# Performance work log

Measured on AMD Instinct MI355X. Metric: run time of the kernel, lower is better.

Reference implementation:

```python
import jax, jax.numpy as jnp
import numpy as np
import math

EMBED = 256
HEADS = 8
HD = EMBED // HEADS  # 32
NB = 3               # n_behaviors
C = NB * NB + 1      # 10 behavior-pair classes
NUM_BUCKETS = 32
MAX_DIST = 40
EPS = 1e-12
B, L = 4, 512


def _rel_bucket(seq_len, num_buckets=NUM_BUCKETS, max_distance=MAX_DIST):
    """T5-style relative position buckets, matching RelativePositionBias._relative_position_bucket."""
    pos = jnp.arange(seq_len)
    relative_position = pos[None, :] - pos[:, None]  # k - q
    n = -relative_position
    nb = num_buckets // 2
    ret = (n < 0).astype(jnp.int32) * nb
    n = jnp.abs(n)
    max_exact = nb // 2
    is_small = n < max_exact
    nf = jnp.maximum(n, 1).astype(jnp.float32)  # clamp to avoid log(0); masked by is_small anyway
    val_large = max_exact + (jnp.log(nf / max_exact) / math.log(max_distance / max_exact) * (nb - max_exact)).astype(jnp.int32)
    val_large = jnp.minimum(val_large, nb - 1)
    return ret + jnp.where(is_small, n, val_large)


def setup_inputs() -> dict:
    key = jax.random.key(0)
    ks = jax.random.split(key, 12)
    s = 0.02
    return {
        "input_tensor": jax.random.normal(ks[0], (B, L, EMBED), jnp.float32),
        "attention_mask": jnp.zeros((B, 1, L, L), jnp.float32),
        "type_seq": jax.random.randint(ks[1], (B, L), 0, NB + 1),
        "Wq": jax.random.normal(ks[2], (NB + 1, EMBED, HEADS, HD), jnp.float32) * s,
        "Wk": jax.random.normal(ks[3], (NB + 1, EMBED, HEADS, HD), jnp.float32) * s,
        "Wv": jax.random.normal(ks[4], (NB + 1, EMBED, HEADS, HD), jnp.float32) * s,
        "W1": jax.random.normal(ks[5], (NB, HEADS, HD, HD), jnp.float32) * s,
        "alpha1": jax.random.normal(ks[6], (C, NB, HEADS), jnp.float32),
        "W2": jax.random.normal(ks[7], (NB, HEADS, HD, HD), jnp.float32) * s,
        "alpha2": jax.random.normal(ks[8], (C, NB, HEADS), jnp.float32),
        "rp_tables": jax.random.normal(ks[9], (C, NUM_BUCKETS, HEADS), jnp.float32) * s,
        "ln_gamma": jnp.ones((EMBED,), jnp.float32),
        "ln_beta": jnp.zeros((EMBED,), jnp.float32),
    }


def reference(input_tensor, attention_mask, type_seq, Wq, Wk, Wv, W1, alpha1, W2, alpha2, rp_tables, ln_gamma, ln_beta):
    bsz, seq_len, emb = input_tensor.shape
    ts = type_seq
    # behavior pair matrix: 0 if either side is padding, else (tq-1)*NB + tk in [1, NB^2]
    bm = ((ts[:, :, None] * ts[:, None, :]) != 0).astype(jnp.int32)
    bm = bm * ((ts[:, :, None] - 1) * NB + ts[:, None, :])  # [B,L,L]

    # --- relative position bias, gathered per behavior pair ---
    bucket = _rel_bucket(seq_len)                 # [L,L]
    vals = rp_tables[:, bucket, :]                # [C,L,L,H]
    qi = jnp.arange(seq_len)[None, :, None]
    ki = jnp.arange(seq_len)[None, None, :]
    bias = vals[bm, qi, ki]                       # [B,L,L,H] gathered along C per pair
    bias = jnp.transpose(bias, (0, 3, 1, 2))      # [B,H,L,L]

    # --- behavior-gated QKV ---
    oh = jax.nn.one_hot(ts, NB + 1, dtype=input_tensor.dtype)  # [B,L,NB+1]
    q = jnp.einsum('BLH,bHhd,BLb->BhLd', input_tensor, Wq, oh)
    k = jnp.einsum('BLH,bHhd,BLb->BhLd', input_tensor, Wk, oh)
    v = jnp.einsum('BLH,bHhd,BLb->BhLd', input_tensor, Wv, oh)

    # --- bilinear scores with per-pair mixing matrices ---
    W1_ = jnp.einsum('bhmn,Cbh->Chmn', W1, jax.nn.softmax(alpha1, axis=1))
    att_all = jnp.einsum('BhQm,Chmn,BhKn->BhQKC', q, W1_, k)  # [B,H,L,L,C]
    scores = jnp.take_along_axis(att_all, bm[:, None, :, :, None], axis=4)[..., 0]
    scores = scores * (1.0 / math.sqrt(HD)) + bias + attention_mask
    probs = jax.nn.softmax(scores, axis=-1)  # dropout=0.0 -> identity

    # --- behavior-mixed value aggregation ---
    W2_ = jnp.einsum('bhmn,Cbh->Chmn', W2, jax.nn.softmax(alpha2, axis=1))
    oh_bm = jax.nn.one_hot(bm, C, dtype=probs.dtype)          # [B,L,L,C]
    pC = probs[:, :, :, :, None] * oh_bm[:, None]             # [B,H,L,L,C]
    ctx = jnp.einsum('BhQKC,Chnm,BhKn->BhQm', pC, W2_, v)     # [B,H,L,d]

    ctx = jnp.transpose(ctx, (0, 2, 1, 3)).reshape(bsz, seq_len, emb)
    x = ctx + input_tensor  # out_dropout=0.0
    mu = jnp.mean(x, axis=-1, keepdims=True)
    var = jnp.mean(jnp.square(x - mu), axis=-1, keepdims=True)
    return (x - mu) / jnp.sqrt(var + EPS) * ln_gamma + ln_beta
```

## Files before the change

### kernel.cpp

```cpp
#include <hip/hip_runtime.h>
#include <math.h>

#define BB 4
#define LL 512
#define EMB 256
#define NH 8
#define HD 32
#define NB_ 3
#define CCN 10
#define NBKT 32
#define SCALE 0.17677669529663687f

typedef __bf16 bf16_t;
typedef __attribute__((ext_vector_type(8))) bf16_t bf16x8;
typedef __attribute__((ext_vector_type(4))) float f32x4;

__device__ __forceinline__ unsigned short f2b(float f) {
    unsigned int u = __float_as_uint(f);
    u += 0x7FFF + ((u >> 16) & 1);
    return (unsigned short)(u >> 16);
}
__device__ __forceinline__ float b2f(unsigned short s) {
    return __uint_as_float(((unsigned int)s) << 16);
}
__device__ __forceinline__ unsigned pack2(float a, float b) {
    return (unsigned)f2b(a) | ((unsigned)f2b(b) << 16);
}
__device__ __forceinline__ int bm_of(int tq, int tk) {
    return (tq * tk != 0) ? ((tq - 1) * 3 + tk) : 0;
}
__device__ __forceinline__ unsigned long long shfl_up64(unsigned long long v, int d) {
    unsigned lo = (unsigned)__shfl_up((int)(unsigned)v, d, 64);
    unsigned hi = (unsigned)__shfl_up((int)(v >> 32), d, 64);
    return (((unsigned long long)hi) << 32) | lo;
}

__device__ __forceinline__ void sort512(const int* __restrict__ tsb, int* spk,
                                        unsigned long long* wtll, int* msc, int tid) {
    int ty0 = tsb[2 * tid], ty1 = tsb[2 * tid + 1];
    unsigned long long pk = (1ULL << (16 * ty0)) + (1ULL << (16 * ty1));
    unsigned long long v = pk;
    int lane = tid & 63;
#pragma unroll
    for (int off = 1; off < 64; off <<= 1) {
        unsigned long long o = shfl_up64(v, off);
        if (lane >= off) v += o;
    }
    int w = tid >> 6;
    if (lane == 63) wtll[w] = v;
    __syncthreads();
    unsigned long long pre = 0, tot = 0;
#pragma unroll
    for (int i = 0; i < 4; i++) {
        unsigned long long xx = wtll[i];
        if (i < w) pre += xx;
        tot += xx;
    }
    v += pre;
    unsigned long long excl = v - pk;
    int c0 = (int)(tot & 0xFFFF), c1 = (int)((tot >> 16) & 0xFFFF);
    int c2 = (int)((tot >> 32) & 0xFFFF), c3 = (int)((tot >> 48) & 0xFFFF);
    int ub0 = 0, ub1 = c0, ub2 = c0 + c1, ub3 = c0 + c1 + c2;
    if (tid == 0) {
        int pc0 = (c0 + 31) & ~31, pc1 = (c1 + 31) & ~31, pc2 = (c2 + 31) & ~31, pc3 = (c3 + 31) & ~31;
        int pb1 = pc0, pb2 = pc0 + pc1, pb3 = pc0 + pc1 + pc2;
        msc[0] = 0;  msc[1] = pb1; msc[2] = pb2; msc[3] = pb3;
        msc[4] = ub0; msc[5] = ub1; msc[6] = ub2; msc[7] = ub3;
        msc[8] = c0; msc[9] = c1; msc[10] = c2; msc[11] = c3;
        msc[12] = (pb3 + pc3 + 63) & ~63;
    }
    int bases[4] = {ub0, ub1, ub2, ub3};
    int r0 = (int)((excl >> (16 * ty0)) & 0xFFFF);
    unsigned long long excl1 = excl + (1ULL << (16 * ty0));
    int r1 = (int)((excl1 >> (16 * ty1)) & 0xFFFF);
    spk[bases[ty0] + r0] = (ty0 << 16) | (2 * tid);
    spk[bases[ty1] + r1] = (ty1 << 16) | (2 * tid + 1);
    __syncthreads();
}

__device__ __forceinline__ void pad_lookup(const int* msc, int pos, int& real, int& upos, int& seg) {
    seg = (pos >= msc[1]) + (pos >= msc[2]) + (pos >= msc[3]);
    int r = pos - msc[seg];
    real = (r < msc[8 + seg]) ? 1 : 0;
    upos = msc[4 + seg] + r;
}

__global__ void k_pre(const float* __restrict__ A1, const float* __restrict__ W1,
                      const float* __restrict__ A2, const float* __restrict__ W2,
                      const float* __restrict__ Wq, const float* __restrict__ Wk, const float* __restrict__ Wv,
                      float* __restrict__ W1s, float* __restrict__ W2s,
                      unsigned short* __restrict__ W1Tb, unsigned short* __restrict__ W2Tb,
                      unsigned short* __restrict__ Wt) {
    __shared__ float cmb[32 * 33];
    __shared__ unsigned short ls[64 * 264];
    int g = blockIdx.x, tid = threadIdx.x;
    if (g < 160) {
        int idx = g;
        const float* alpha = (idx < 80) ? A1 : A2;
        const float* W     = (idx < 80) ? W1 : W2;
        float* Ws          = (idx < 80) ? W1s : W2s;
        unsigned short* WT = (idx < 80) ? W1Tb : W2Tb;
        idx %= 80;
        int cc = idx / NH, h = idx % NH;
        float a0 = alpha[cc * NB_ * NH + 0 * NH + h];
        float a1 = alpha[cc * NB_ * NH + 1 * NH + h];
        float a2 = alpha[cc * NB_ * NH + 2 * NH + h];
        float mx = fmaxf(a0, fmaxf(a1, a2));
        float e0 = __expf(a0 - mx), e1 = __expf(a1 - mx), e2 = __expf(a2 - mx);
        float inv = 1.0f / (e0 + e1 + e2);
        e0 *= inv; e1 *= inv; e2 *= inv;
        for (int i = tid; i < HD * HD; i += 256) {
            int m = i >> 5, n = i & 31;
            float acc = e0 * W[((0 * NH + h) * HD + m) * HD + n]
                      + e1 * W[((1 * NH + h) * HD + m) * HD + n]
                      + e2 * W[((2 * NH + h) * HD + m) * HD + n];
            cmb[m * 33 + n] = acc;
        }
        __syncthreads();
        for (int i = tid; i < HD * HD; i += 256) {
            int a = i >> 5, bq = i & 31;
            Ws[((cc * NH + h) * HD + a) * HD + bq] = cmb[a * 33 + bq];
            WT[((size_t)(cc * NH + h) * HD + a) * HD + bq] = f2b(cmb[bq * 33 + a]);
        }
        return;
    }
    int t = g - 160;
    int tw = t >> 2, ob = t & 3;
    int which = tw >> 2, ty = tw & 3;
    const float* src = ((which == 0) ? Wq : (which == 1) ? Wk : Wv) + (size_t)ty * EMB * EMB;
    int out0 = ob * 64;
    for (int it = 0; it < 16; it++) {
        int e = it * 16 + (tid >> 4);
        int o4 = (tid & 15) * 4;
        float4 v = *(const float4*)&src[(size_t)e * EMB + out0 + o4];
        ls[(o4 + 0) * 264 + e] = f2b(v.x);
        ls[(o4 + 1) * 264 + e] = f2b(v.y);
        ls[(o4 + 2) * 264 + e] = f2b(v.z);
        ls[(o4 + 3) * 264 + e] = f2b(v.w);
    }
    __syncthreads();
    int out = tid >> 2, ech = (tid & 3) * 8;
    unsigned short* dst = Wt + (size_t)tw * EMB * EMB + (size_t)(out0 + out) * EMB;
    const unsigned short* srcl = &ls[out * 264];
#pragma unroll
    for (int jj = 0; jj < 8; jj++)
        *(uint4*)&dst[ech + jj * 32] = *(const uint4*)&srcl[ech + jj * 32];
}

__global__ __launch_bounds__(256, 4) void k_qkv(
    const float* __restrict__ x, const int* __restrict__ ts,
    const unsigned short* __restrict__ Wt,
    float* __restrict__ qp, float* __restrict__ kp, float* __restrict__ vp) {
    __shared__ int spk[LL];
    __shared__ unsigned long long wtll[4];
    __shared__ int msc[16];
    __shared__ unsigned short xs[32 * 264];
    __shared__ unsigned short wt[128 * 72];

    int g = blockIdx.x, tid = threadIdx.x;
    int ns = g % 6, gb = g / 6;
    int b = gb >> 4, tb = gb & 15, i0 = tb * 32;
    int which = ns >> 1, nh = ns & 1;
    int wave = tid >> 6, lane = tid & 63, quad = lane >> 4, col = lane & 15;

    sort512(ts + b * LL, spk, wtll, msc, tid);

    {
        int tok = tid >> 3, e32 = (tid & 7) * 32;
        int tok_orig = spk[i0 + tok] & 0xFFFF;
        const float* src = &x[(size_t)(b * LL + tok_orig) * EMB + e32];
        unsigned short* dstl = &xs[tok * 264 + e32];
#pragma unroll
        for (int jj = 0; jj < 4; jj++) {
            float4 v0 = *(const float4*)&src[jj * 8];
            float4 v1 = *(const float4*)&src[jj * 8 + 4];
            uint4 w;
            w.x = pack2(v0.x, v0.y); w.y = pack2(v0.z, v0.w);
            w.z = pack2(v1.x, v1.y); w.w = pack2(v1.z, v1.w);
            *(uint4*)&dstl[jj * 8] = w;
        }
    }
    int t_start = spk[i0] >> 16, t_end = spk[i0 + 31] >> 16;
    float* outp = (which == 0) ? qp : (which == 1) ? kp : vp;

    for (int ty = t_start; ty <= t_end; ty++) {
        f32x4 acc[2][2];
#pragma unroll
        for (int mt = 0; mt < 2; mt++)
#pragma unroll
            for (int nt = 0; nt < 2; nt++) acc[mt][nt] = (f32x4){0.f, 0.f, 0.f, 0.f};
        const unsigned short* wsrc = Wt + (size_t)(which * 4 + ty) * EMB * EMB + (size_t)(nh * 128) * EMB;
        for (int c = 0; c < 4; c++) {
            {
                int outloc = tid >> 1, e32 = (tid & 1) * 32;
                const unsigned short* srcw = &wsrc[(size_t)outloc * EMB + c * 64 + e32];
                unsigned short* dstw = &wt[outloc * 72 + e32];
#pragma unroll
                for (int jj = 0; jj < 4; jj++)
                    *(uint4*)&dstw[jj * 8] = *(const uint4*)&srcw[jj * 8];
            }
            __syncthreads();
#pragma unroll
            for (int kk = 0; kk < 2; kk++) {
                bf16x8 a0 = *(const bf16x8*)&xs[(0 * 16 + col) * 264 + c * 64 + kk * 32 + quad * 8];
                bf16x8 a1 = *(const bf16x8*)&xs[(1 * 16 + col) * 264 + c * 64 + kk * 32 + quad * 8];
                bf16x8 b0 = *(const bf16x8*)&wt[((wave * 2 + 0) * 16 + col) * 72 + kk * 32 + quad * 8];
                bf16x8 b1 = *(const bf16x8*)&wt[((wave * 2 + 1) * 16 + col) * 72 + kk * 32 + quad * 8];
                acc[0][0] = __builtin_amdgcn_mfma_f32_16x16x32_bf16(a0, b0, acc[0][0], 0, 0, 0);
                acc[0][1] = __builtin_amdgcn_mfma_f32_16x16x32_bf16(a0, b1, acc[0][1], 0, 0, 0);
                acc[1][0] = __builtin_amdgcn_mfma_f32_16x16x32_bf16(a1, b0, acc[1][0], 0, 0, 0);
                acc[1][1] = __builtin_amdgcn_mfma_f32_16x16x32_bf16(a1, b1, acc[1][1], 0, 0, 0);
            }
            __syncthreads();
        }
#pragma unroll
        for (int mt = 0; mt < 2; mt++)
#pragma unroll
            for (int r = 0; r < 4; r++) {
                int tokloc = mt * 16 + quad * 4 + r;
                int tty = spk[i0 + tokloc] >> 16;
                if (tty != ty) continue;
#pragma unroll
                for (int nt = 0; nt < 2; nt++) {
                    int n = nh * 128 + (wave * 2 + nt) * 16 + col;
                    int h = n >> 5, d = n & 31;
                    outp[((size_t)(b * NH + h) * LL + i0 + tokloc) * HD + d] = acc[mt][nt][r];
                }
            }
    }
}

#define SCP 648
#define OFF_UN   20736
#define OFF_QTB  29184
#define OFF_KPAD 33536
#define OFF_TBL  36096
#define OFF_RPL  37120
#define OFF_WT   38400
#define OFF_QOR  38432
#define OFF_QTY  38496
#define OFF_INV  38560
#define OFF_MSC  38624
#define SM_TOTAL 38688
__global__ __launch_bounds__(256, 4) void k_attn(
    const float* __restrict__ qp, const float* __restrict__ kp, const float* __restrict__ vp,
    const int* __restrict__ ts, const float* __restrict__ rp, const float* __restrict__ am,
    const float* __restrict__ W1s, const float* __restrict__ W2s,
    const unsigned short* __restrict__ W1Tb, const unsigned short* __restrict__ W2Tb,
    float* __restrict__ ctx) {
    __shared__ __align__(16) char smem[SM_TOTAL];
    unsigned short* scu = (unsigned short*)smem;
    int*   spk  = (int*)smem;
    unsigned short* qstb = (unsigned short*)(smem + OFF_UN);
    unsigned short* kbuf = (unsigned short*)(smem + OFF_UN);
    unsigned short* vt   = (unsigned short*)(smem + OFF_UN);
    float* sb   = (float*)(smem + OFF_UN);
    unsigned short* qtb = (unsigned short*)(smem + OFF_QTB);
    unsigned short* sbb = (unsigned short*)(smem + OFF_QTB);
    int*   kpad = (int*)(smem + OFF_KPAD);
    short* tbl  = (short*)(smem + OFF_TBL);
    float* rp_l = (float*)(smem + OFF_RPL);
    unsigned long long* wtll = (unsigned long long*)(smem + OFF_WT);
    int*   qor_l = (int*)(smem + OFF_QOR);
    int*   qty_l = (int*)(smem + OFF_QTY);
    float* inv_l = (float*)(smem + OFF_INV);
    int*   msc   = (int*)(smem + OFF_MSC);

    int blk = blockIdx.x;
    int b = blk >> 8, h = (blk >> 5) & 7, q16 = blk & 31;
    int i0q = q16 * 16;
    int tid = threadIdx.x;
    int wave = tid >> 6, lane = tid & 63, quad = lane >> 4, col = lane & 15;
    int bh = b * NH + h;

    for (int d = tid; d < LL; d += 256) {
        int v;
        if (d < 8) v = d;
        else {
            double r = log((double)d / 8.0) / log(5.0);
            v = 8 + (int)(r * 8.0);
            if (v > 15) v = 15;
        }
        tbl[d] = (short)v;
    }
    for (int i = tid; i < CCN * NBKT; i += 256) rp_l[i] = rp[i * NH + h];

    sort512(ts + b * LL, spk, wtll, msc, tid);

    int KT = msc[12];
    if (tid < 16) {
        int v = spk[i0q + tid];
        qor_l[tid] = v & 0xFFFF; qty_l[tid] = v >> 16;
    }
    for (int pos = tid; pos < KT; pos += 256) {
        int real, upos, seg;
        pad_lookup(msc, pos, real, upos, seg);
        kpad[pos] = real ? spk[upos] : ((seg << 16) | 0xFFFF);
    }
    {
        int q = tid >> 4, m2 = (tid & 15) * 2;
        const float* src = &qp[((size_t)bh * LL + i0q + q) * HD + m2];
        ((unsigned*)qstb)[q * 20 + (tid & 15)] = pack2(src[0], src[1]);
    }
    __syncthreads();

    int qor_r[4], qty_r[4];
#pragma unroll
    for (int r = 0; r < 4; r++) { qor_r[r] = qor_l[quad * 4 + r]; qty_r[r] = qty_l[quad * 4 + r]; }
    bool uniq = (qty_l[0] == qty_l[15]);
    int tqu = qty_l[0];

    if (uniq) {
#pragma unroll
        for (int it = 0; it < 2; it++) {
            int t8 = wave * 2 + it;
            int tk = t8 >> 1, nhf = t8 & 1;
            int bmv = bm_of(tqu, tk);
            bf16x8 a = *(const bf16x8*)&qstb[col * 40 + quad * 8];
            bf16x8 bb = *(const bf16x8*)&W1Tb[((size_t)(bmv * NH + h) * HD + nhf * 16 + col) * HD + quad * 8];
            f32x4 d = {0.f, 0.f, 0.f, 0.f};
            d = __builtin_amdgcn_mfma_f32_16x16x32_bf16(a, bb, d, 0, 0, 0);
#pragma unroll
            for (int r = 0; r < 4; r++)
                qtb[(quad * 4 + r) * 136 + tk * 32 + nhf * 16 + col] = f2b(d[r]);
        }
    } else {
        for (int i = tid; i < 16 * 128; i += 256) {
            int q = i >> 7, r = i & 127, tk = r >> 5, n = r & 31;
            int bmv = bm_of(qty_l[q], tk);
            const float* wb = &W1s[((bmv * NH + h) * HD) * HD + n];
            float acc = 0.f;
#pragma unroll
            for (int m = 0; m < HD; m++) acc += b2f(qstb[q * 40 + m]) * wb[m * HD];
            qtb[q * 136 + tk * 32 + n] = f2b(acc);
        }
    }
    __syncthreads();

    const float* amb = am + (size_t)b * LL * LL;
    for (int kt0 = 0; kt0 < KT; kt0 += 64) {
        {
            int kk = tid >> 2, m8 = (tid & 3) * 8;
            int real, upos, seg;
            pad_lookup(msc, kt0 + kk, real, upos, seg);
            uint4 w = make_uint4(0, 0, 0, 0);
            if (real) {
                const float4* src = (const float4*)&kp[((size_t)bh * LL + upos) * HD + m8];
                float4 v0 = src[0], v1 = src[1];
                w.x = pack2(v0.x, v0.y); w.y = pack2(v0.z, v0.w);
                w.z = pack2(v1.x, v1.y); w.w = pack2(v1.z, v1.w);
            }
            *(uint4*)&kbuf[kk * 40 + m8] = w;
        }
        __syncthreads();
        {
            int kb = kt0 + wave * 16;
            int tk = kpad[kb] >> 16;
            bf16x8 a = *(const bf16x8*)&qtb[col * 136 + tk * 32 + quad * 8];
            bf16x8 bfr = *(const bf16x8*)&kbuf[(wave * 16 + col) * 40 + quad * 8];
            f32x4 d = {0.f, 0.f, 0.f, 0.f};
            d = __builtin_amdgcn_mfma_f32_16x16x32_bf16(a, bfr, d, 0, 0, 0);
            int kpi = kb + col;
            int kv = kpad[kpi];
            int ko = kv & 0xFFFF;
            if (ko == 0xFFFF) {
#pragma unroll
                for (int r = 0; r < 4; r++) scu[(quad * 4 + r) * SCP + kpi] = 0xFF80;
            } else {
                int tkk = kv >> 16;
#pragma unroll
                for (int r = 0; r < 4; r++) {
                    int q = quad * 4 + r;
                    int qo = qor_r[r];
                    int dd = qo - ko;
                    int ad = dd < 0 ? -dd : dd;
                    int bk = (dd < 0 ? 16 : 0) + (int)tbl[ad];
                    float bias = rp_l[bm_of(qty_r[r], tkk) * NBKT + bk];
                    float mval = amb[(size_t)qo * LL + ko];
                    scu[q * SCP + kpi] = f2b(d[r] * SCALE + bias + mval);
                }
            }
        }
        __syncthreads();
    }

    {
        int gq = tid >> 4, t16 = tid & 15;
        float mx = -1e30f;
        for (int kk = t16; kk < KT; kk += 16) mx = fmaxf(mx, b2f(scu[gq * SCP + kk]));
#pragma unroll
        for (int off = 1; off < 16; off <<= 1) mx = fmaxf(mx, __shfl_xor(mx, off, 16));
        float sum = 0.f;
        for (int kk = t16; kk < KT; kk += 16) {
            int idx = gq * SCP + kk;
            float e = __expf(b2f(scu[idx]) - mx);
            scu[idx] = f2b(e); sum += e;
        }
#pragma unroll
        for (int off = 1; off < 16; off <<= 1) sum += __shfl_xor(sum, off, 16);
        if (t16 == 0) inv_l[gq] = 1.0f / sum;
    }
    __syncthreads();

    f32x4 accv[4][2];
#pragma unroll
    for (int t = 0; t < 4; t++)
#pragma unroll
        for (int hh = 0; hh < 2; hh++) accv[t][hh] = (f32x4){0.f, 0.f, 0.f, 0.f};

    for (int kt0 = 0; kt0 < KT; kt0 += 64) {
        {
            int kk = tid >> 2, n8 = (tid & 3) * 8;
            int real, upos, seg;
            pad_lookup(msc, kt0 + kk, real, upos, seg);
            float vv[8] = {0, 0, 0, 0, 0, 0, 0, 0};
            if (real) {
                const float4* src = (const float4*)&vp[((size_t)bh * LL + upos) * HD + n8];
                float4 v0 = src[0], v1 = src[1];
                vv[0] = v0.x; vv[1] = v0.y; vv[2] = v0.z; vv[3] = v0.w;
                vv[4] = v1.x; vv[5] = v1.y; vv[6] = v1.z; vv[7] = v1.w;
            }
#pragma unroll
            for (int i = 0; i < 8; i++) {
                int n = n8 + i;
                int ph = ((n & 3) << 3) | (n >> 2);
                vt[ph * 72 + kk] = f2b(vv[i]);
            }
        }
        __syncthreads();
        int c = kt0 >> 6;
        int g0 = 2 * c;
        int pc = ((col & 3) << 3) | (col >> 2);
#pragma unroll
        for (int gl = 0; gl < 2; gl++) {
            int g = g0 + gl;
            if ((g & 3) != wave) continue;
            int loc = gl * 32;
            int tk = kpad[kt0 + loc] >> 16;
            bf16x8 a = *(const bf16x8*)&scu[col * SCP + kt0 + loc + quad * 8];
            bf16x8 b0 = *(const bf16x8*)&vt[pc * 72 + loc + quad * 8];
            bf16x8 b1 = *(const bf16x8*)&vt[(pc + 4) * 72 + loc + quad * 8];
            if (tk == 0) {
                accv[0][0] = __builtin_amdgcn_mfma_f32_16x16x32_bf16(a, b0, accv[0][0], 0, 0, 0);
                accv[0][1] = __builtin_amdgcn_mfma_f32_16x16x32_bf16(a, b1, accv[0][1], 0, 0, 0);
            } else if (tk == 1) {
                accv[1][0] = __builtin_amdgcn_mfma_f32_16x16x32_bf16(a, b0, accv[1][0], 0, 0, 0);
                accv[1][1] = __builtin_amdgcn_mfma_f32_16x16x32_bf16(a, b1, accv[1][1], 0, 0, 0);
            } else if (tk == 2) {
                accv[2][0] = __builtin_amdgcn_mfma_f32_16x16x32_bf16(a, b0, accv[2][0], 0, 0, 0);
                accv[2][1] = __builtin_amdgcn_mfma_f32_16x16x32_bf16(a, b1, accv[2][1], 0, 0, 0);
            } else {
                accv[3][0] = __builtin_amdgcn_mfma_f32_16x16x32_bf16(a, b0, accv[3][0], 0, 0, 0);
                accv[3][1] = __builtin_amdgcn_mfma_f32_16x16x32_bf16(a, b1, accv[3][1], 0, 0, 0);
            }
        }
        __syncthreads();
    }

#pragma unroll
    for (int w = 0; w < 4; w++) {
        if (wave == w) {
#pragma unroll
            for (int t = 0; t < 4; t++)
#pragma unroll
                for (int hh = 0; hh < 2; hh++)
#pragma unroll
                    for (int r = 0; r < 4; r++) {
                        int q = quad * 4 + r;
                        int n = col + 16 * hh;
                        float val = accv[t][hh][r];
                        if (w == 0) {
                            sb[q * 132 + t * 32 + n] = val;
                        } else if (w < 3) {
                            sb[q * 132 + t * 32 + n] += val;
                        } else {
                            float fin = sb[q * 132 + t * 32 + n] + val;
                            sb[q * 132 + t * 32 + n] = fin;
                            sbb[q * 136 + t * 32 + n] = f2b(fin);
                        }
                    }
        }
        __syncthreads();
    }

    if (uniq) {
        if (wave < 2) {
            int mhf = wave;
            f32x4 d = {0.f, 0.f, 0.f, 0.f};
#pragma unroll
            for (int tk = 0; tk < 4; tk++) {
                int bmv = bm_of(tqu, tk);
                bf16x8 a = *(const bf16x8*)&sbb[col * 136 + tk * 32 + quad * 8];
                bf16x8 bb = *(const bf16x8*)&W2Tb[((size_t)(bmv * NH + h) * HD + mhf * 16 + col) * HD + quad * 8];
                d = __builtin_amdgcn_mfma_f32_16x16x32_bf16(a, bb, d, 0, 0, 0);
            }
#pragma unroll
            for (int r = 0; r < 4; r++) {
                int q = quad * 4 + r;
                ctx[((size_t)(b * LL + qor_l[q])) * EMB + h * HD + mhf * 16 + col] = d[r] * inv_l[q];
            }
        }
    } else {
        int m = tid & 31, qq = tid >> 5;
#pragma unroll
        for (int rep = 0; rep < 2; rep++) {
            int qi = qq + 8 * rep;
            int tq = qty_l[qi];
            float acc = 0.f;
#pragma unroll
            for (int tk2 = 0; tk2 < 4; tk2++) {
                int bmv = bm_of(tq, tk2);
                const float* wb = &W2s[((bmv * NH + h) * HD) * HD + m];
                const float* sbp = &sb[qi * 132 + tk2 * 32];
                for (int n = 0; n < HD; n++) acc += sbp[n] * wb[n * HD];
            }
            int qo = qor_l[qi];
            ctx[((size_t)(b * LL + qo)) * EMB + h * HD + m] = acc * inv_l[qi];
        }
    }
}

__global__ void k_ln(const float* __restrict__ ctx, const float* __restrict__ x,
                     const float* __restrict__ gamma, const float* __restrict__ beta,
                     float* __restrict__ out) {
    __shared__ float red[8];
    __shared__ float red2[8];
    int blk = blockIdx.x;
    int b = blk >> 9, l = blk & 511;
    int j = threadIdx.x;
    size_t base = ((size_t)(b * LL + l)) * EMB;
    float v = ctx[base + j] + x[base + j];
    float s = v, s2 = v * v;
    for (int off = 32; off > 0; off >>= 1) { s += __shfl_down(s, off, 64); s2 += __shfl_down(s2, off, 64); }
    int wid = j >> 6;
    if ((j & 63) == 0) { red[wid] = s; red2[wid] = s2; }
    __syncthreads();
    if (j == 0) {
        float ts_ = 0, ts2 = 0;
        for (int w = 0; w < 4; w++) { ts_ += red[w]; ts2 += red2[w]; }
        red[4] = ts_; red2[4] = ts2;
    }
    __syncthreads();
    float mu = red[4] / (float)EMB;
    float var = red2[4] / (float)EMB - mu * mu;
    float r = rsqrtf(var + 1e-12f);
    out[base + j] = (v - mu) * r * gamma[j] + beta[j];
}

extern "C" void kernel_launch(void* const* d_in, const int* in_sizes, int n_in,
                              void* d_out, int out_size, void* d_ws, size_t ws_size,
                              hipStream_t stream) {
    const float* x  = (const float*)d_in[0];
    const float* am = (const float*)d_in[1];
    const int*   ts = (const int*)d_in[2];
    const float* Wq = (const float*)d_in[3];
    const float* Wk = (const float*)d_in[4];
    const float* Wv = (const float*)d_in[5];
    const float* W1 = (const float*)d_in[6];
    const float* a1 = (const float*)d_in[7];
    const float* W2 = (const float*)d_in[8];
    const float* a2 = (const float*)d_in[9];
    const float* rp = (const float*)d_in[10];
    const float* g  = (const float*)d_in[11];
    const float* be = (const float*)d_in[12];
    float* out = (float*)d_out;

    float* ws  = (float*)d_ws;
    float* W1s = ws;
    float* W2s = ws + 81920;
    unsigned short* W1Tb = (unsigned short*)(ws + 163840);
    unsigned short* W2Tb = (unsigned short*)(ws + 204800);
    float* qp  = ws + 245760;
    float* kp  = qp + BB * NH * LL * HD;
    float* vp  = kp + BB * NH * LL * HD;
    float* ctx = vp + BB * NH * LL * HD;
    unsigned short* Wt = (unsigned short*)ctx;

    hipLaunchKernelGGL(k_pre, dim3(208), dim3(256), 0, stream,
                       a1, W1, a2, W2, Wq, Wk, Wv, W1s, W2s, W1Tb, W2Tb, Wt);
    hipLaunchKernelGGL(k_qkv, dim3(384), dim3(256), 0, stream, x, ts, Wt, qp, kp, vp);
    hipLaunchKernelGGL(k_attn, dim3(BB * NH * 32), dim3(256), 0, stream,
                       qp, kp, vp, ts, rp, am, W1s, W2s, W1Tb, W2Tb, ctx);
    hipLaunchKernelGGL(k_ln, dim3(BB * LL), dim3(256), 0, stream, ctx, x, g, be, out);
}
```

Baseline: 139.9 us.

## Store Q/K/V as bf16, skip zero attention mask, drop LDS staging

Q, K and V projections are now written as bf16 instead of fp32, which halves their global traffic and removes repacking in the attention kernel. The prep kernel gets 256 extra blocks that scan the attention mask and set a device flag when any value is nonzero, so the attention kernel can skip mask loads when the mask is all zero. The QKV GEMM now loads A fragments into registers and B directly from global, removing LDS staging and barriers. The score loop is restructured so each wave handles its own key tiles without per-tile block syncs, and fully padded tiles are skipped. Padded-key metadata is packed into a single int per key.

```diff
diff --git a/kernel.cpp b/kernel.cpp
--- a/kernel.cpp
+++ b/kernel.cpp
@@ -88,9 +88,10 @@
 __global__ void k_pre(const float* __restrict__ A1, const float* __restrict__ W1,
                       const float* __restrict__ A2, const float* __restrict__ W2,
                       const float* __restrict__ Wq, const float* __restrict__ Wk, const float* __restrict__ Wv,
+                      const float* __restrict__ am,
                       float* __restrict__ W1s, float* __restrict__ W2s,
                       unsigned short* __restrict__ W1Tb, unsigned short* __restrict__ W2Tb,
-                      unsigned short* __restrict__ Wt) {
+                      unsigned short* __restrict__ Wt, int* __restrict__ mflag) {
     __shared__ float cmb[32 * 33];
     __shared__ unsigned short ls[64 * 264];
     int g = blockIdx.x, tid = threadIdx.x;
@@ -124,38 +125,50 @@
         }
         return;
     }
-    int t = g - 160;
-    int tw = t >> 2, ob = t & 3;
-    int which = tw >> 2, ty = tw & 3;
-    const float* src = ((which == 0) ? Wq : (which == 1) ? Wk : Wv) + (size_t)ty * EMB * EMB;
-    int out0 = ob * 64;
-    for (int it = 0; it < 16; it++) {
-        int e = it * 16 + (tid >> 4);
-        int o4 = (tid & 15) * 4;
-        float4 v = *(const float4*)&src[(size_t)e * EMB + out0 + o4];
-        ls[(o4 + 0) * 264 + e] = f2b(v.x);
-        ls[(o4 + 1) * 264 + e] = f2b(v.y);
-        ls[(o4 + 2) * 264 + e] = f2b(v.z);
-        ls[(o4 + 3) * 264 + e] = f2b(v.w);
-    }
-    __syncthreads();
-    int out = tid >> 2, ech = (tid & 3) * 8;
-    unsigned short* dst = Wt + (size_t)tw * EMB * EMB + (size_t)(out0 + out) * EMB;
-    const unsigned short* srcl = &ls[out * 264];
-#pragma unroll
-    for (int jj = 0; jj < 8; jj++)
-        *(uint4*)&dst[ech + jj * 32] = *(const uint4*)&srcl[ech + jj * 32];
+    if (g < 208) {
+        int t = g - 160;
+        int tw = t >> 2, ob = t & 3;
+        int which = tw >> 2, ty = tw & 3;
+        const float* src = ((which == 0) ? Wq : (which == 1) ? Wk : Wv) + (size_t)ty * EMB * EMB;
+        int out0 = ob * 64;
+        for (int it = 0; it < 16; it++) {
+            int e = it * 16 + (tid >> 4);
+            int o4 = (tid & 15) * 4;
+            float4 v = *(const float4*)&src[(size_t)e * EMB + out0 + o4];
+            ls[(o4 + 0) * 264 + e] = f2b(v.x);
+            ls[(o4 + 1) * 264 + e] = f2b(v.y);
+            ls[(o4 + 2) * 264 + e] = f2b(v.z);
+            ls[(o4 + 3) * 264 + e] = f2b(v.w);
+        }
+        __syncthreads();
+        int out = tid >> 2, ech = (tid & 3) * 8;
+        unsigned short* dst = Wt + (size_t)tw * EMB * EMB + (size_t)(out0 + out) * EMB;
+        const unsigned short* srcl = &ls[out * 264];
+#pragma unroll
+        for (int jj = 0; jj < 8; jj++)
+            *(uint4*)&dst[ech + jj * 32] = *(const uint4*)&srcl[ech + jj * 32];
+        return;
+    }
+    {
+        int idx = g - 208;
+        const uint4* p = (const uint4*)am + (size_t)idx * 1024;
+        unsigned o = 0;
+#pragma unroll
+        for (int j = 0; j < 4; j++) {
+            uint4 v = p[tid + j * 256];
+            o |= v.x | v.y | v.z | v.w;
+        }
+        if (o) atomicOr(mflag, 1);
+    }
 }
 
 __global__ __launch_bounds__(256, 4) void k_qkv(
     const float* __restrict__ x, const int* __restrict__ ts,
     const unsigned short* __restrict__ Wt,
-    float* __restrict__ qp, float* __restrict__ kp, float* __restrict__ vp) {
+    unsigned short* __restrict__ qp, unsigned short* __restrict__ kp, unsigned short* __restrict__ vp) {
     __shared__ int spk[LL];
     __shared__ unsigned long long wtll[4];
     __shared__ int msc[16];
-    __shared__ unsigned short xs[32 * 264];
-    __shared__ unsigned short wt[128 * 72];
 
     int g = blockIdx.x, tid = threadIdx.x;
     int ns = g % 6, gb = g / 6;
@@ -165,23 +178,23 @@
 
     sort512(ts + b * LL, spk, wtll, msc, tid);
 
-    {
-        int tok = tid >> 3, e32 = (tid & 7) * 32;
-        int tok_orig = spk[i0 + tok] & 0xFFFF;
-        const float* src = &x[(size_t)(b * LL + tok_orig) * EMB + e32];
-        unsigned short* dstl = &xs[tok * 264 + e32];
-#pragma unroll
-        for (int jj = 0; jj < 4; jj++) {
-            float4 v0 = *(const float4*)&src[jj * 8];
-            float4 v1 = *(const float4*)&src[jj * 8 + 4];
-            uint4 w;
-            w.x = pack2(v0.x, v0.y); w.y = pack2(v0.z, v0.w);
-            w.z = pack2(v1.x, v1.y); w.w = pack2(v1.z, v1.w);
-            *(uint4*)&dstl[jj * 8] = w;
+    bf16x8 afr[2][8];
+#pragma unroll
+    for (int mt = 0; mt < 2; mt++) {
+        int orig = spk[i0 + mt * 16 + col] & 0xFFFF;
+        const float* xr = &x[(size_t)(b * LL + orig) * EMB];
+#pragma unroll
+        for (int kc = 0; kc < 8; kc++) {
+            float4 v0 = *(const float4*)&xr[kc * 32 + quad * 8];
+            float4 v1 = *(const float4*)&xr[kc * 32 + quad * 8 + 4];
+            uint4 up;
+            up.x = pack2(v0.x, v0.y); up.y = pack2(v0.z, v0.w);
+            up.z = pack2(v1.x, v1.y); up.w = pack2(v1.z, v1.w);
+            afr[mt][kc] = *(bf16x8*)&up;
         }
     }
     int t_start = spk[i0] >> 16, t_end = spk[i0 + 31] >> 16;
-    float* outp = (which == 0) ? qp : (which == 1) ? kp : vp;
+    unsigned short* outp = (which == 0) ? qp : (which == 1) ? kp : vp;
 
     for (int ty = t_start; ty <= t_end; ty++) {
         f32x4 acc[2][2];
@@ -190,28 +203,16 @@
 #pragma unroll
             for (int nt = 0; nt < 2; nt++) acc[mt][nt] = (f32x4){0.f, 0.f, 0.f, 0.f};
         const unsigned short* wsrc = Wt + (size_t)(which * 4 + ty) * EMB * EMB + (size_t)(nh * 128) * EMB;
-        for (int c = 0; c < 4; c++) {
-            {
-                int outloc = tid >> 1, e32 = (tid & 1) * 32;
-                const unsigned short* srcw = &wsrc[(size_t)outloc * EMB + c * 64 + e32];
-                unsigned short* dstw = &wt[outloc * 72 + e32];
-#pragma unroll
-                for (int jj = 0; jj < 4; jj++)
-                    *(uint4*)&dstw[jj * 8] = *(const uint4*)&srcw[jj * 8];
-            }
-            __syncthreads();
-#pragma unroll
-            for (int kk = 0; kk < 2; kk++) {
-                bf16x8 a0 = *(const bf16x8*)&xs[(0 * 16 + col) * 264 + c * 64 + kk * 32 + quad * 8];
-                bf16x8 a1 = *(const bf16x8*)&xs[(1 * 16 + col) * 264 + c * 64 + kk * 32 + quad * 8];
-                bf16x8 b0 = *(const bf16x8*)&wt[((wave * 2 + 0) * 16 + col) * 72 + kk * 32 + quad * 8];
-                bf16x8 b1 = *(const bf16x8*)&wt[((wave * 2 + 1) * 16 + col) * 72 + kk * 32 + quad * 8];
-                acc[0][0] = __builtin_amdgcn_mfma_f32_16x16x32_bf16(a0, b0, acc[0][0], 0, 0, 0);
-                acc[0][1] = __builtin_amdgcn_mfma_f32_16x16x32_bf16(a0, b1, acc[0][1], 0, 0, 0);
-                acc[1][0] = __builtin_amdgcn_mfma_f32_16x16x32_bf16(a1, b0, acc[1][0], 0, 0, 0);
-                acc[1][1] = __builtin_amdgcn_mfma_f32_16x16x32_bf16(a1, b1, acc[1][1], 0, 0, 0);
-            }
-            __syncthreads();
+        const unsigned short* w0 = &wsrc[(size_t)((wave * 2 + 0) * 16 + col) * EMB + quad * 8];
+        const unsigned short* w1 = &wsrc[(size_t)((wave * 2 + 1) * 16 + col) * EMB + quad * 8];
+#pragma unroll
+        for (int kc = 0; kc < 8; kc++) {
+            bf16x8 b0 = *(const bf16x8*)&w0[kc * 32];
+            bf16x8 b1 = *(const bf16x8*)&w1[kc * 32];
+            acc[0][0] = __builtin_amdgcn_mfma_f32_16x16x32_bf16(afr[0][kc], b0, acc[0][0], 0, 0, 0);
+            acc[0][1] = __builtin_amdgcn_mfma_f32_16x16x32_bf16(afr[0][kc], b1, acc[0][1], 0, 0, 0);
+            acc[1][0] = __builtin_amdgcn_mfma_f32_16x16x32_bf16(afr[1][kc], b0, acc[1][0], 0, 0, 0);
+            acc[1][1] = __builtin_amdgcn_mfma_f32_16x16x32_bf16(afr[1][kc], b1, acc[1][1], 0, 0, 0);
         }
 #pragma unroll
         for (int mt = 0; mt < 2; mt++)
@@ -224,7 +225,7 @@
                 for (int nt = 0; nt < 2; nt++) {
                     int n = nh * 128 + (wave * 2 + nt) * 16 + col;
                     int h = n >> 5, d = n & 31;
-                    outp[((size_t)(b * NH + h) * LL + i0 + tokloc) * HD + d] = acc[mt][nt][r];
+                    outp[((size_t)(b * NH + h) * LL + i0 + tokloc) * HD + d] = f2b(acc[mt][nt][r]);
                 }
             }
     }
@@ -243,16 +244,16 @@
 #define OFF_MSC  38624
 #define SM_TOTAL 38688
 __global__ __launch_bounds__(256, 4) void k_attn(
-    const float* __restrict__ qp, const float* __restrict__ kp, const float* __restrict__ vp,
+    const unsigned short* __restrict__ qp, const unsigned short* __restrict__ kp,
+    const unsigned short* __restrict__ vp,
     const int* __restrict__ ts, const float* __restrict__ rp, const float* __restrict__ am,
     const float* __restrict__ W1s, const float* __restrict__ W2s,
     const unsigned short* __restrict__ W1Tb, const unsigned short* __restrict__ W2Tb,
-    float* __restrict__ ctx) {
+    const int* __restrict__ mflag, float* __restrict__ ctx) {
     __shared__ __align__(16) char smem[SM_TOTAL];
     unsigned short* scu = (unsigned short*)smem;
     int*   spk  = (int*)smem;
     unsigned short* qstb = (unsigned short*)(smem + OFF_UN);
-    unsigned short* kbuf = (unsigned short*)(smem + OFF_UN);
     unsigned short* vt   = (unsigned short*)(smem + OFF_UN);
     float* sb   = (float*)(smem + OFF_UN);
     unsigned short* qtb = (unsigned short*)(smem + OFF_QTB);
@@ -272,6 +273,7 @@
     int tid = threadIdx.x;
     int wave = tid >> 6, lane = tid & 63, quad = lane >> 4, col = lane & 15;
     int bh = b * NH + h;
+    int mz = (mflag[0] == 0);
 
     for (int d = tid; d < LL; d += 256) {
         int v;
@@ -295,12 +297,13 @@
     for (int pos = tid; pos < KT; pos += 256) {
         int real, upos, seg;
         pad_lookup(msc, pos, real, upos, seg);
-        kpad[pos] = real ? spk[upos] : ((seg << 16) | 0xFFFF);
+        int orig = real ? (spk[upos] & 0xFFFF) : 0x3FF;
+        kpad[pos] = (seg << 20) | ((real ? upos : 0) << 10) | orig;
     }
     {
         int q = tid >> 4, m2 = (tid & 15) * 2;
-        const float* src = &qp[((size_t)bh * LL + i0q + q) * HD + m2];
-        ((unsigned*)qstb)[q * 20 + (tid & 15)] = pack2(src[0], src[1]);
+        ((unsigned*)qstb)[q * 20 + (tid & 15)] =
+            *(const unsigned*)&qp[((size_t)bh * LL + i0q + q) * HD + m2];
     }
     __syncthreads();
 
@@ -338,51 +341,45 @@
     __syncthreads();
 
     const float* amb = am + (size_t)b * LL * LL;
-    for (int kt0 = 0; kt0 < KT; kt0 += 64) {
-        {
-            int kk = tid >> 2, m8 = (tid & 3) * 8;
-            int real, upos, seg;
-            pad_lookup(msc, kt0 + kk, real, upos, seg);
-            uint4 w = make_uint4(0, 0, 0, 0);
-            if (real) {
-                const float4* src = (const float4*)&kp[((size_t)bh * LL + upos) * HD + m8];
-                float4 v0 = src[0], v1 = src[1];
-                w.x = pack2(v0.x, v0.y); w.y = pack2(v0.z, v0.w);
-                w.z = pack2(v1.x, v1.y); w.w = pack2(v1.z, v1.w);
-            }
-            *(uint4*)&kbuf[kk * 40 + m8] = w;
-        }
-        __syncthreads();
-        {
-            int kb = kt0 + wave * 16;
-            int tk = kpad[kb] >> 16;
-            bf16x8 a = *(const bf16x8*)&qtb[col * 136 + tk * 32 + quad * 8];
-            bf16x8 bfr = *(const bf16x8*)&kbuf[(wave * 16 + col) * 40 + quad * 8];
-            f32x4 d = {0.f, 0.f, 0.f, 0.f};
-            d = __builtin_amdgcn_mfma_f32_16x16x32_bf16(a, bfr, d, 0, 0, 0);
-            int kpi = kb + col;
-            int kv = kpad[kpi];
-            int ko = kv & 0xFFFF;
-            if (ko == 0xFFFF) {
-#pragma unroll
-                for (int r = 0; r < 4; r++) scu[(quad * 4 + r) * SCP + kpi] = 0xFF80;
-            } else {
-                int tkk = kv >> 16;
-#pragma unroll
-                for (int r = 0; r < 4; r++) {
-                    int q = quad * 4 + r;
-                    int qo = qor_r[r];
-                    int dd = qo - ko;
-                    int ad = dd < 0 ? -dd : dd;
-                    int bk = (dd < 0 ? 16 : 0) + (int)tbl[ad];
-                    float bias = rp_l[bm_of(qty_r[r], tkk) * NBKT + bk];
-                    float mval = amb[(size_t)qo * LL + ko];
-                    scu[q * SCP + kpi] = f2b(d[r] * SCALE + bias + mval);
-                }
-            }
-        }
-        __syncthreads();
-    }
+    int ntiles = KT >> 4;
+    for (int tile = wave; tile < ntiles; tile += 4) {
+        int kb = tile * 16;
+        int kv0 = kpad[kb];
+        if ((kv0 & 0x3FF) == 0x3FF) {
+#pragma unroll
+            for (int r = 0; r < 4; r++) scu[(quad * 4 + r) * SCP + kb + col] = 0xFF80;
+            continue;
+        }
+        int tkt = kv0 >> 20;
+        int kpi = kb + col;
+        int kv = kpad[kpi];
+        int ko = kv & 0x3FF;
+        int upos = (kv >> 10) & 0x3FF;
+        bool real = (ko != 0x3FF);
+        bf16x8 bfr;
+        if (real) bfr = *(const bf16x8*)&kp[((size_t)bh * LL + upos) * HD + quad * 8];
+        else { uint4 z = make_uint4(0, 0, 0, 0); bfr = *(bf16x8*)&z; }
+        bf16x8 a = *(const bf16x8*)&qtb[col * 136 + tkt * 32 + quad * 8];
+        f32x4 d = {0.f, 0.f, 0.f, 0.f};
+        d = __builtin_amdgcn_mfma_f32_16x16x32_bf16(a, bfr, d, 0, 0, 0);
+        if (!real) {
+#pragma unroll
+            for (int r = 0; r < 4; r++) scu[(quad * 4 + r) * SCP + kpi] = 0xFF80;
+        } else {
+#pragma unroll
+            for (int r = 0; r < 4; r++) {
+                int q = quad * 4 + r;
+                int qo = qor_r[r];
+                int dd = qo - ko;
+                int ad = dd < 0 ? -dd : dd;
+                int bk = (dd < 0 ? 16 : 0) + (int)tbl[ad];
+                float sv = d[r] * SCALE + rp_l[bm_of(qty_r[r], tkt) * NBKT + bk];
+                if (!mz) sv += amb[(size_t)qo * LL + ko];
+                scu[q * SCP + kpi] = f2b(sv);
+            }
+        }
+    }
+    __syncthreads();
 
     {
         int gq = tid >> 4, t16 = tid & 15;
@@ -411,20 +408,21 @@
     for (int kt0 = 0; kt0 < KT; kt0 += 64) {
         {
             int kk = tid >> 2, n8 = (tid & 3) * 8;
-            int real, upos, seg;
-            pad_lookup(msc, kt0 + kk, real, upos, seg);
-            float vv[8] = {0, 0, 0, 0, 0, 0, 0, 0};
-            if (real) {
-                const float4* src = (const float4*)&vp[((size_t)bh * LL + upos) * HD + n8];
-                float4 v0 = src[0], v1 = src[1];
-                vv[0] = v0.x; vv[1] = v0.y; vv[2] = v0.z; vv[3] = v0.w;
-                vv[4] = v1.x; vv[5] = v1.y; vv[6] = v1.z; vv[7] = v1.w;
-            }
+            int kv = kpad[kt0 + kk];
+            int upos = (kv >> 10) & 0x3FF;
+            bool real = ((kv & 0x3FF) != 0x3FF);
+            uint4 w = make_uint4(0, 0, 0, 0);
+            if (real) w = *(const uint4*)&vp[((size_t)bh * LL + upos) * HD + n8];
+            unsigned short sv[8] = {
+                (unsigned short)(w.x & 0xFFFF), (unsigned short)(w.x >> 16),
+                (unsigned short)(w.y & 0xFFFF), (unsigned short)(w.y >> 16),
+                (unsigned short)(w.z & 0xFFFF), (unsigned short)(w.z >> 16),
+                (unsigned short)(w.w & 0xFFFF), (unsigned short)(w.w >> 16)};
 #pragma unroll
             for (int i = 0; i < 8; i++) {
                 int n = n8 + i;
                 int ph = ((n & 3) << 3) | (n >> 2);
-                vt[ph * 72 + kk] = f2b(vv[i]);
+                vt[ph * 72 + kk] = sv[i];
             }
         }
         __syncthreads();
@@ -433,10 +431,12 @@
         int pc = ((col & 3) << 3) | (col >> 2);
 #pragma unroll
         for (int gl = 0; gl < 2; gl++) {
-            int g = g0 + gl;
-            if ((g & 3) != wave) continue;
+            int gg = g0 + gl;
+            if ((gg & 3) != wave) continue;
             int loc = gl * 32;
-            int tk = kpad[kt0 + loc] >> 16;
+            int kvg = kpad[kt0 + loc];
+            if ((kvg & 0x3FF) == 0x3FF) continue;
+            int tk = kvg >> 20;
             bf16x8 a = *(const bf16x8*)&scu[col * SCP + kt0 + loc + quad * 8];
             bf16x8 b0 = *(const bf16x8*)&vt[pc * 72 + loc + quad * 8];
             bf16x8 b1 = *(const bf16x8*)&vt[(pc + 4) * 72 + loc + quad * 8];
@@ -570,16 +570,18 @@
     float* W2s = ws + 81920;
     unsigned short* W1Tb = (unsigned short*)(ws + 163840);
     unsigned short* W2Tb = (unsigned short*)(ws + 204800);
-    float* qp  = ws + 245760;
-    float* kp  = qp + BB * NH * LL * HD;
-    float* vp  = kp + BB * NH * LL * HD;
-    float* ctx = vp + BB * NH * LL * HD;
+    int* mflag = (int*)(ws + 245760);
+    unsigned short* qp = (unsigned short*)(ws + 245776);
+    unsigned short* kp = qp + BB * NH * LL * HD;
+    unsigned short* vp = kp + BB * NH * LL * HD;
+    float* ctx = (float*)(vp + BB * NH * LL * HD);
     unsigned short* Wt = (unsigned short*)ctx;
 
-    hipLaunchKernelGGL(k_pre, dim3(208), dim3(256), 0, stream,
-                       a1, W1, a2, W2, Wq, Wk, Wv, W1s, W2s, W1Tb, W2Tb, Wt);
+    hipMemsetAsync(mflag, 0, 4, stream);
+    hipLaunchKernelGGL(k_pre, dim3(464), dim3(256), 0, stream,
+                       a1, W1, a2, W2, Wq, Wk, Wv, am, W1s, W2s, W1Tb, W2Tb, Wt, mflag);
     hipLaunchKernelGGL(k_qkv, dim3(384), dim3(256), 0, stream, x, ts, Wt, qp, kp, vp);
     hipLaunchKernelGGL(k_attn, dim3(BB * NH * 32), dim3(256), 0, stream,
-                       qp, kp, vp, ts, rp, am, W1s, W2s, W1Tb, W2Tb, ctx);
+                       qp, kp, vp, ts, rp, am, W1s, W2s, W1Tb, W2Tb, mflag, ctx);
     hipLaunchKernelGGL(k_ln, dim3(BB * LL), dim3(256), 0, stream, ctx, x, g, be, out);
 }
```

After: 144.6 us. +3.4%, slower.
